# Performance work log

Measured on AMD Instinct MI355X. Metric: run time of the kernel, lower is better.

The kernel has to match this reference:

```python
import jax, jax.numpy as jnp
import numpy as np

BS, SEQ, DIM, HEADS = 2, 2048, 1024, 16
HEAD_DIM = DIM // HEADS
NEG = -1e9


def setup_inputs() -> dict:
    key = jax.random.key(0)
    ks = jax.random.split(key, 5)
    s = 1.0 / np.sqrt(DIM)
    return {
        "x": jax.random.normal(ks[0], (BS, SEQ, DIM), jnp.float32),
        "padding_mask": jnp.ones((BS, SEQ), jnp.int32),
        "causal_mask": jnp.tril(jnp.ones((SEQ, SEQ), jnp.int32)),
        "Wq": jax.random.normal(ks[1], (DIM, DIM), jnp.float32) * s,
        "bq": jnp.zeros((DIM,), jnp.float32),
        "Wk": jax.random.normal(ks[2], (DIM, DIM), jnp.float32) * s,
        "bk": jnp.zeros((DIM,), jnp.float32),
        "Wv": jax.random.normal(ks[3], (DIM, DIM), jnp.float32) * s,
        "bv": jnp.zeros((DIM,), jnp.float32),
        "Wo": jax.random.normal(ks[4], (DIM, DIM), jnp.float32) * s,
        "bo": jnp.zeros((DIM,), jnp.float32),
    }


def reference(x, padding_mask, causal_mask, Wq, bq, Wk, bk, Wv, bv, Wo, bo):
    bs, seq, dim = x.shape
    # QKV projections -> [b, h, s, d]
    def proj(W, b):
        return (x @ W.T + b).reshape(bs, seq, HEADS, HEAD_DIM).transpose(0, 2, 1, 3)
    q, k, v = proj(Wq, bq), proj(Wk, bk), proj(Wv, bv)
    scores = jnp.einsum("bhqd,bhkd->bhqk", q, k) / np.sqrt(HEAD_DIM).astype(np.float32)
    scores = jnp.where(padding_mask[:, None, None, :] == 0, NEG, scores)
    scores = jnp.where(causal_mask[None, None, :, :] == 0, NEG, scores)
    attn = jax.nn.softmax(scores, axis=-1)
    out = jnp.einsum("bhqk,bhkd->bhqd", attn, v)
    out = out.transpose(0, 2, 1, 3).reshape(bs, seq, dim)
    return out @ Wo.T + bo
```

## Files before the change

### kernel.cpp

```cpp
#include <hip/hip_runtime.h>
#include <hip/hip_bf16.h>
#include <stdint.h>

#define SEQ 2048
#define DIM 1024
#define HEADS 16
#define HD 64
#define NEGV (-1e9f)
#define SCALE2 0.18033688011112042f
#define THR2 11.541560327111707f

typedef __attribute__((ext_vector_type(8))) short short8;
typedef __attribute__((ext_vector_type(4))) float f32x4;

__device__ __forceinline__ unsigned short f2bf(float f) {
  __hip_bfloat16 h = __float2bfloat16(f);
  union { __hip_bfloat16 h; unsigned short u; } cv;
  cv.h = h;
  return cv.u;
}

__device__ __forceinline__ void async16(const void* g, void* l) {
  __builtin_amdgcn_global_load_lds(
      (const __attribute__((address_space(1))) unsigned int*)g,
      (__attribute__((address_space(3))) unsigned int*)l, 16, 0, 0);
}

__global__ void cast_bf16_k(const float* __restrict__ in,
                            unsigned short* __restrict__ out, int n4) {
  int stride = gridDim.x * blockDim.x;
  for (int i = blockIdx.x * blockDim.x + threadIdx.x; i < n4; i += stride) {
    float4 v = ((const float4*)in)[i];
    ushort4 o;
    o.x = f2bf(v.x); o.y = f2bf(v.y); o.z = f2bf(v.z); o.w = f2bf(v.w);
    ((ushort4*)out)[i] = o;
  }
}

__global__ void cast_w4_k(const float* __restrict__ w0, const float* __restrict__ w1,
                          const float* __restrict__ w2, const float* __restrict__ w3,
                          unsigned short* __restrict__ o0, unsigned short* __restrict__ o1,
                          unsigned short* __restrict__ o2, unsigned short* __restrict__ o3,
                          int n4) {
  const float* in = (blockIdx.y == 0) ? w0 : (blockIdx.y == 1) ? w1
                   : (blockIdx.y == 2) ? w2 : w3;
  unsigned short* out = (blockIdx.y == 0) ? o0 : (blockIdx.y == 1) ? o1
                       : (blockIdx.y == 2) ? o2 : o3;
  int stride = gridDim.x * blockDim.x;
  for (int i = blockIdx.x * blockDim.x + threadIdx.x; i < n4; i += stride) {
    float4 v = ((const float4*)in)[i];
    ushort4 o;
    o.x = f2bf(v.x); o.y = f2bf(v.y); o.z = f2bf(v.z); o.w = f2bf(v.w);
    ((ushort4*)out)[i] = o;
  }
}

__device__ __forceinline__ void stage_ab(const unsigned short* __restrict__ A,
                                         const unsigned short* __restrict__ B,
                                         int K, int bm0, int bn0, int k0,
                                         unsigned short* As, unsigned short* Bs,
                                         int tid) {
#pragma unroll
  for (int i = 0; i < 2; ++i) {
    int e   = (i * 256 + tid) * 8;
    int row = e >> 5;
    int kk  = e & 31;
    async16(A + (size_t)(bm0 + row) * K + (size_t)(k0 + kk), As + e);
    async16(B + (size_t)(bn0 + row) * K + (size_t)(k0 + kk), Bs + e);
  }
}

__device__ __forceinline__ void gemm_core(const unsigned short* __restrict__ A,
                                          const unsigned short* __restrict__ B,
                                          int K, int bm0, int bn0,
                                          unsigned short (*As)[128 * 32],
                                          unsigned short (*Bs)[128 * 32],
                                          f32x4 acc[4][4]) {
  const int tid  = threadIdx.x;
  const int lane = tid & 63;
  const int w    = tid >> 6;
  const int wr   = w >> 1, wc = w & 1;
  const int lrow = lane & 15, lkg = lane >> 4;

  stage_ab(A, B, K, bm0, bn0, 0, As[0], Bs[0], tid);
  __syncthreads();

  for (int k0 = 0; k0 < K; k0 += 32) {
    const int cur = (k0 >> 5) & 1;
    if (k0 + 32 < K)
      stage_ab(A, B, K, bm0, bn0, k0 + 32, As[cur ^ 1], Bs[cur ^ 1], tid);

    short8 af[4], bf[4];
#pragma unroll
    for (int i = 0; i < 4; ++i) {
      af[i] = *(const short8*)(As[cur] + (wr * 64 + i * 16 + lrow) * 32 + lkg * 8);
      bf[i] = *(const short8*)(Bs[cur] + (wc * 64 + i * 16 + lrow) * 32 + lkg * 8);
    }
#pragma unroll
    for (int i = 0; i < 4; ++i)
#pragma unroll
      for (int j = 0; j < 4; ++j)
        acc[i][j] = __builtin_amdgcn_mfma_f32_16x16x32_bf16(af[i], bf[j], acc[i][j], 0, 0, 0);

    __syncthreads();
  }
}

__global__ __launch_bounds__(256)
void qkv_gemm_k(const unsigned short* __restrict__ xb,
                const unsigned short* __restrict__ wqb,
                const unsigned short* __restrict__ wkb,
                const unsigned short* __restrict__ wvb,
                const float* __restrict__ bq, const float* __restrict__ bk,
                const float* __restrict__ bv,
                unsigned short* __restrict__ Qb, unsigned short* __restrict__ Kb,
                unsigned short* __restrict__ Vtb) {
  __shared__ __align__(16) unsigned short As[2][128 * 32];
  __shared__ __align__(16) unsigned short Bs[2][128 * 32];
  const int z = blockIdx.z;
  const unsigned short* B = (z == 0) ? wqb : (z == 1) ? wkb : wvb;
  const float* bias       = (z == 0) ? bq  : (z == 1) ? bk  : bv;
  const int bm0 = blockIdx.y * 128, bn0 = blockIdx.x * 128;

  f32x4 acc[4][4] = {};
  gemm_core(xb, B, DIM, bm0, bn0, As, Bs, acc);

  const int lane = threadIdx.x & 63;
  const int w = threadIdx.x >> 6, wr = w >> 1, wc = w & 1;
  unsigned short* out01 = (z == 0) ? Qb : Kb;
#pragma unroll
  for (int i = 0; i < 4; ++i)
#pragma unroll
    for (int j = 0; j < 4; ++j)
#pragma unroll
      for (int r = 0; r < 4; ++r) {
        int mg = bm0 + wr * 64 + i * 16 + (lane >> 4) * 4 + r;
        int ng = bn0 + wc * 64 + j * 16 + (lane & 15);
        float v = acc[i][j][r] + bias[ng];
        int bb = mg >> 11, s = mg & 2047, h = ng >> 6, d = ng & 63;
        int bh = bb * HEADS + h;
        if (z < 2)
          out01[((size_t)bh * SEQ + s) * HD + d] = f2bf(v);
        else
          Vtb[((size_t)bh * HD + d) * SEQ + s] = f2bf(v);
      }
}

__global__ __launch_bounds__(256)
void out_gemm_k(const unsigned short* __restrict__ Ob,
                const unsigned short* __restrict__ wob,
                const float* __restrict__ bo, float* __restrict__ out) {
  __shared__ __align__(16) unsigned short As[2][128 * 32];
  __shared__ __align__(16) unsigned short Bs[2][128 * 32];
  const int bm0 = blockIdx.y * 128, bn0 = blockIdx.x * 128;

  f32x4 acc[4][4] = {};
  gemm_core(Ob, wob, DIM, bm0, bn0, As, Bs, acc);

  const int lane = threadIdx.x & 63;
  const int w = threadIdx.x >> 6, wr = w >> 1, wc = w & 1;
#pragma unroll
  for (int i = 0; i < 4; ++i)
#pragma unroll
    for (int j = 0; j < 4; ++j)
#pragma unroll
      for (int r = 0; r < 4; ++r) {
        int mg = bm0 + wr * 64 + i * 16 + (lane >> 4) * 4 + r;
        int ng = bn0 + wc * 64 + j * 16 + (lane & 15);
        out[(size_t)mg * DIM + ng] = acc[i][j][r] + bo[ng];
      }
}

__device__ __forceinline__ void stage_kv64(const unsigned short* __restrict__ kbase,
                                           const unsigned short* __restrict__ vbase,
                                           int k0, unsigned short* KsB,
                                           unsigned short* VsB, int tid) {
#pragma unroll
  for (int j = 0; j < 2; ++j) {
    const int c    = j * 256 + tid;
    const int row  = c >> 3;
    const int colb = (c & 7) << 4;
    const int srcb = colb ^ ((row & 7) << 4);
    async16(kbase + (size_t)(k0 + row) * HD + (srcb >> 1), KsB + c * 8);
  }
#pragma unroll
  for (int j = 0; j < 2; ++j) {
    const int c    = j * 256 + tid;
    const int d    = c >> 3;
    const int colb = (c & 7) << 4;
    const int srcb = colb ^ ((d & 7) << 4);
    async16(vbase + (size_t)d * SEQ + k0 + (srcb >> 1), VsB + c * 8);
  }
}

__global__ __launch_bounds__(256)
void attn_k(const unsigned short* __restrict__ Q,
            const unsigned short* __restrict__ Kp,
            const unsigned short* __restrict__ Vt,
            const int* __restrict__ pm,
            unsigned short* __restrict__ O) {
  __shared__ __align__(16) unsigned short Ks[2][64 * 64];
  __shared__ __align__(16) unsigned short Vs[2][64 * 64];
  __shared__ __align__(16) unsigned short plds[4][16 * 64];

  const int tid  = threadIdx.x;
  const int lane = tid & 63;
  const int w    = tid >> 6;
  const int lc = lane & 15, lg = lane >> 4;
  const int y = blockIdx.y;
  const int r_ = y & 7, m_ = y >> 3;
  const int qb = (m_ == 0) ? r_ : (m_ == 1) ? (15 - r_)
               : (m_ == 2) ? (16 + r_) : (31 - r_);
  const int bh = blockIdx.x;
  const int b  = bh >> 4, h = bh & 15;

  const size_t base = (size_t)bh * SEQ * HD;
  const unsigned short* kbase = Kp + base;
  const unsigned short* vbase = Vt + (size_t)bh * HD * SEQ;
  const int* pmb = pm + b * SEQ;
  char* pb = (char*)&plds[w][0];
  const int swp = (lc & 7) << 4;

  const int qrow0 = qb * 64 + w * 16;
  const int qrow  = qrow0 + lc;

  short8 qa[2];
  {
    const unsigned short* qp = Q + base + (size_t)qrow * HD + lg * 8;
    qa[0] = *(const short8*)(qp);
    qa[1] = *(const short8*)(qp + 32);
  }

  f32x4 oacc[4] = {};
  float mrow = -1e30f, lsum = 0.f;

  const int nk = qb + 1;

  stage_kv64(kbase, vbase, 0, Ks[0], Vs[0], tid);

  int ok = 1;
  for (int i = lane; i < SEQ / 4; i += 64) {
    int4 v = ((const int4*)pmb)[i];
    ok &= (v.x != 0) & (v.y != 0) & (v.z != 0) & (v.w != 0);
  }
  const bool allones = __all(ok);
  __syncthreads();

  for (int kt = 0; kt < nk; ++kt) {
    const int cur = kt & 1;
    const int k0 = kt * 64;
    if (kt + 1 < nk)
      stage_kv64(kbase, vbase, k0 + 64, Ks[cur ^ 1], Vs[cur ^ 1], tid);

    f32x4 s[4];
    const char* kbuf = (const char*)Ks[cur];
    __builtin_amdgcn_s_setprio(1);
#pragma unroll
    for (int t = 0; t < 4; ++t) {
      const int row = t * 16 + lc;
      const int swk = (row & 7) << 4;
      const char* kr = kbuf + row * 128;
      short8 kb0 = *(const short8*)(kr + ((lg * 16) ^ swk));
      short8 kb1 = *(const short8*)(kr + ((lg * 16 + 64) ^ swk));
      f32x4 z = {};
      z = __builtin_amdgcn_mfma_f32_16x16x32_bf16(kb0, qa[0], z, 0, 0, 0);
      z = __builtin_amdgcn_mfma_f32_16x16x32_bf16(kb1, qa[1], z, 0, 0, 0);
#pragma unroll
      for (int r = 0; r < 4; ++r) s[t][r] = z[r] * SCALE2;
    }
    __builtin_amdgcn_s_setprio(0);

    if (!allones) {
#pragma unroll
      for (int t = 0; t < 4; ++t) {
        const int kr0 = k0 + t * 16;
        int4 pmv = *(const int4*)(pmb + kr0 + lg * 4);
#pragma unroll
        for (int r = 0; r < 4; ++r) {
          const int kidx = kr0 + lg * 4 + r;
          if (kidx > qrow || (&pmv.x)[r] == 0) s[t][r] = NEGV;
        }
      }
    } else if (kt == qb) {
#pragma unroll
      for (int t = 0; t < 4; ++t)
#pragma unroll
        for (int r = 0; r < 4; ++r) {
          const int kidx = k0 + t * 16 + lg * 4 + r;
          if (kidx > qrow) s[t][r] = NEGV;
        }
    }

    float mx = -1e30f;
#pragma unroll
    for (int t = 0; t < 4; ++t)
      mx = fmaxf(mx, fmaxf(fmaxf(s[t][0], s[t][1]), fmaxf(s[t][2], s[t][3])));
    if (!__all(mx <= mrow + THR2)) {
      mx = fmaxf(mx, __shfl_xor(mx, 16, 64));
      mx = fmaxf(mx, __shfl_xor(mx, 32, 64));
      const float mnew = fmaxf(mrow, mx);
      const float sc = exp2f(mrow - mnew);
      lsum *= sc;
      mrow = mnew;
      const float s0 = __shfl(sc, lg * 4 + 0, 64);
      const float s1 = __shfl(sc, lg * 4 + 1, 64);
      const float s2 = __shfl(sc, lg * 4 + 2, 64);
      const float s3 = __shfl(sc, lg * 4 + 3, 64);
#pragma unroll
      for (int t = 0; t < 4; ++t) {
        oacc[t][0] *= s0; oacc[t][1] *= s1; oacc[t][2] *= s2; oacc[t][3] *= s3;
      }
    }
    float sum = 0.f;
#pragma unroll
    for (int t = 0; t < 4; ++t)
#pragma unroll
      for (int r = 0; r < 4; ++r) {
        const float p = exp2f(s[t][r] - mrow);
        s[t][r] = p;
        sum += p;
      }
    lsum += sum;

#pragma unroll
    for (int t = 0; t < 4; ++t) {
      short4 pk;
      pk.x = (short)f2bf(s[t][0]); pk.y = (short)f2bf(s[t][1]);
      pk.z = (short)f2bf(s[t][2]); pk.w = (short)f2bf(s[t][3]);
      const int colb = (t * 16 + lg * 4) * 2;
      *(short4*)(pb + lc * 128 + (colb ^ swp)) = pk;
    }
    short8 pa[2];
#pragma unroll
    for (int ks = 0; ks < 2; ++ks)
      pa[ks] = *(const short8*)(pb + lc * 128 + (((ks * 32 + lg * 8) * 2) ^ swp));

    const char* vbuf = (const char*)Vs[cur];
    __builtin_amdgcn_s_setprio(1);
#pragma unroll
    for (int t = 0; t < 4; ++t) {
      const int d = t * 16 + lc;
      const int swv = (d & 7) << 4;
      const char* vr = vbuf + d * 128;
#pragma unroll
      for (int ks = 0; ks < 2; ++ks) {
        short8 vv = *(const short8*)(vr + ((ks * 64 + lg * 16) ^ swv));
        oacc[t] = __builtin_amdgcn_mfma_f32_16x16x32_bf16(pa[ks], vv, oacc[t], 0, 0, 0);
      }
    }
    __builtin_amdgcn_s_setprio(0);

    __syncthreads();
  }

  lsum += __shfl_xor(lsum, 16, 64);
  lsum += __shfl_xor(lsum, 32, 64);
  const float l0 = __shfl(lsum, lg * 4 + 0, 64);
  const float l1 = __shfl(lsum, lg * 4 + 1, 64);
  const float l2 = __shfl(lsum, lg * 4 + 2, 64);
  const float l3 = __shfl(lsum, lg * 4 + 3, 64);
  const float i0 = 1.f / l0, i1 = 1.f / l1, i2 = 1.f / l2, i3 = 1.f / l3;
#pragma unroll
  for (int t = 0; t < 4; ++t) {
    const size_t o0 = ((size_t)(b * SEQ + qrow0 + lg * 4)) * DIM + h * HD + t * 16 + lc;
    O[o0]           = f2bf(oacc[t][0] * i0);
    O[o0 + DIM]     = f2bf(oacc[t][1] * i1);
    O[o0 + 2 * DIM] = f2bf(oacc[t][2] * i2);
    O[o0 + 3 * DIM] = f2bf(oacc[t][3] * i3);
  }
}

extern "C" void kernel_launch(void* const* d_in, const int* in_sizes, int n_in,
                              void* d_out, int out_size, void* d_ws, size_t ws_size,
                              hipStream_t stream) {
  const float* x  = (const float*)d_in[0];
  const int*   pm = (const int*)d_in[1];
  const float* Wq = (const float*)d_in[3];
  const float* bq = (const float*)d_in[4];
  const float* Wk = (const float*)d_in[5];
  const float* bk = (const float*)d_in[6];
  const float* Wv = (const float*)d_in[7];
  const float* bv = (const float*)d_in[8];
  const float* Wo = (const float*)d_in[9];
  const float* bo = (const float*)d_in[10];

  const size_t NX = (size_t)4096 * 1024;
  const size_t NW = (size_t)1024 * 1024;

  unsigned short* ws  = (unsigned short*)d_ws;
  unsigned short* xb  = ws;
  unsigned short* wqb = xb + NX;
  unsigned short* wkb = wqb + NW;
  unsigned short* wvb = wkb + NW;
  unsigned short* wob = wvb + NW;
  unsigned short* Qb  = wob + NW;
  unsigned short* Kb  = Qb + NX;
  unsigned short* Vtb = Kb + NX;
  unsigned short* Ob  = xb;

  cast_bf16_k<<<dim3(2048), dim3(256), 0, stream>>>(x, xb, (int)(NX / 4));
  cast_w4_k<<<dim3(512, 4), dim3(256), 0, stream>>>(Wq, Wk, Wv, Wo,
                                                    wqb, wkb, wvb, wob,
                                                    (int)(NW / 4));

  qkv_gemm_k<<<dim3(8, 32, 3), dim3(256), 0, stream>>>(xb, wqb, wkb, wvb,
                                                       bq, bk, bv, Qb, Kb, Vtb);

  attn_k<<<dim3(32, 32), dim3(256), 0, stream>>>(Qb, Kb, Vtb, pm, Ob);

  out_gemm_k<<<dim3(8, 32), dim3(256), 0, stream>>>(Ob, wob, bo, (float*)d_out);
}
```

Baseline: 131.7 us.

## Use 128-key attention tiles, merge cast kernels, and reorder query blocks

Attention now stages and processes 128 keys per iteration instead of 64. This roughly halves the loop trips and barriers and gives each wave more MFMA work between syncs. In exchange it doubles LDS for the K/V/P buffers, which can lower occupancy, and it wastes masked compute on the diagonal tile when the query-block index is even. Query blocks are now scheduled heaviest-first (descending) instead of in the interleaved order. The x and weight fp32-to-bf16 casts are merged into one launch to save launch overhead.

```diff
diff --git a/kernel.cpp b/kernel.cpp
--- a/kernel.cpp
+++ b/kernel.cpp
@@ -26,26 +26,19 @@
       (__attribute__((address_space(3))) unsigned int*)l, 16, 0, 0);
 }
 
-__global__ void cast_bf16_k(const float* __restrict__ in,
-                            unsigned short* __restrict__ out, int n4) {
-  int stride = gridDim.x * blockDim.x;
-  for (int i = blockIdx.x * blockDim.x + threadIdx.x; i < n4; i += stride) {
-    float4 v = ((const float4*)in)[i];
-    ushort4 o;
-    o.x = f2bf(v.x); o.y = f2bf(v.y); o.z = f2bf(v.z); o.w = f2bf(v.w);
-    ((ushort4*)out)[i] = o;
-  }
-}
-
-__global__ void cast_w4_k(const float* __restrict__ w0, const float* __restrict__ w1,
-                          const float* __restrict__ w2, const float* __restrict__ w3,
-                          unsigned short* __restrict__ o0, unsigned short* __restrict__ o1,
-                          unsigned short* __restrict__ o2, unsigned short* __restrict__ o3,
-                          int n4) {
-  const float* in = (blockIdx.y == 0) ? w0 : (blockIdx.y == 1) ? w1
-                   : (blockIdx.y == 2) ? w2 : w3;
-  unsigned short* out = (blockIdx.y == 0) ? o0 : (blockIdx.y == 1) ? o1
-                       : (blockIdx.y == 2) ? o2 : o3;
+__global__ void cast_all_k(const float* __restrict__ x,
+                           const float* __restrict__ w0, const float* __restrict__ w1,
+                           const float* __restrict__ w2, const float* __restrict__ w3,
+                           unsigned short* __restrict__ xo,
+                           unsigned short* __restrict__ o0, unsigned short* __restrict__ o1,
+                           unsigned short* __restrict__ o2, unsigned short* __restrict__ o3,
+                           int nx4, int nw4) {
+  const int seg = blockIdx.y;
+  const float* in = (seg == 0) ? x : (seg == 1) ? w0 : (seg == 2) ? w1
+                   : (seg == 3) ? w2 : w3;
+  unsigned short* out = (seg == 0) ? xo : (seg == 1) ? o0 : (seg == 2) ? o1
+                       : (seg == 3) ? o2 : o3;
+  const int n4 = (seg == 0) ? nx4 : nw4;
   int stride = gridDim.x * blockDim.x;
   for (int i = blockIdx.x * blockDim.x + threadIdx.x; i < n4; i += stride) {
     float4 v = ((const float4*)in)[i];
@@ -171,12 +164,12 @@
       }
 }
 
-__device__ __forceinline__ void stage_kv64(const unsigned short* __restrict__ kbase,
-                                           const unsigned short* __restrict__ vbase,
-                                           int k0, unsigned short* KsB,
-                                           unsigned short* VsB, int tid) {
-#pragma unroll
-  for (int j = 0; j < 2; ++j) {
+__device__ __forceinline__ void stage_kv128(const unsigned short* __restrict__ kbase,
+                                            const unsigned short* __restrict__ vbase,
+                                            int k0, unsigned short* KsB,
+                                            unsigned short* VsB, int tid) {
+#pragma unroll
+  for (int j = 0; j < 4; ++j) {
     const int c    = j * 256 + tid;
     const int row  = c >> 3;
     const int colb = (c & 7) << 4;
@@ -184,10 +177,10 @@
     async16(kbase + (size_t)(k0 + row) * HD + (srcb >> 1), KsB + c * 8);
   }
 #pragma unroll
-  for (int j = 0; j < 2; ++j) {
+  for (int j = 0; j < 4; ++j) {
     const int c    = j * 256 + tid;
-    const int d    = c >> 3;
-    const int colb = (c & 7) << 4;
+    const int d    = c >> 4;
+    const int colb = (c & 15) << 4;
     const int srcb = colb ^ ((d & 7) << 4);
     async16(vbase + (size_t)d * SEQ + k0 + (srcb >> 1), VsB + c * 8);
   }
@@ -199,18 +192,15 @@
             const unsigned short* __restrict__ Vt,
             const int* __restrict__ pm,
             unsigned short* __restrict__ O) {
-  __shared__ __align__(16) unsigned short Ks[2][64 * 64];
-  __shared__ __align__(16) unsigned short Vs[2][64 * 64];
-  __shared__ __align__(16) unsigned short plds[4][16 * 64];
+  __shared__ __align__(16) unsigned short Ks[2][128 * 64];
+  __shared__ __align__(16) unsigned short Vs[2][64 * 128];
+  __shared__ __align__(16) unsigned short plds[4][16 * 128];
 
   const int tid  = threadIdx.x;
   const int lane = tid & 63;
   const int w    = tid >> 6;
   const int lc = lane & 15, lg = lane >> 4;
-  const int y = blockIdx.y;
-  const int r_ = y & 7, m_ = y >> 3;
-  const int qb = (m_ == 0) ? r_ : (m_ == 1) ? (15 - r_)
-               : (m_ == 2) ? (16 + r_) : (31 - r_);
+  const int qb = 31 - blockIdx.y;
   const int bh = blockIdx.x;
   const int b  = bh >> 4, h = bh & 15;
 
@@ -234,9 +224,9 @@
   f32x4 oacc[4] = {};
   float mrow = -1e30f, lsum = 0.f;
 
-  const int nk = qb + 1;
-
-  stage_kv64(kbase, vbase, 0, Ks[0], Vs[0], tid);
+  const int nk = (qb + 2) >> 1;
+
+  stage_kv128(kbase, vbase, 0, Ks[0], Vs[0], tid);
 
   int ok = 1;
   for (int i = lane; i < SEQ / 4; i += 64) {
@@ -248,15 +238,15 @@
 
   for (int kt = 0; kt < nk; ++kt) {
     const int cur = kt & 1;
-    const int k0 = kt * 64;
+    const int k0 = kt * 128;
     if (kt + 1 < nk)
-      stage_kv64(kbase, vbase, k0 + 64, Ks[cur ^ 1], Vs[cur ^ 1], tid);
-
-    f32x4 s[4];
+      stage_kv128(kbase, vbase, k0 + 128, Ks[cur ^ 1], Vs[cur ^ 1], tid);
+
+    f32x4 s[8];
     const char* kbuf = (const char*)Ks[cur];
     __builtin_amdgcn_s_setprio(1);
 #pragma unroll
-    for (int t = 0; t < 4; ++t) {
+    for (int t = 0; t < 8; ++t) {
       const int row = t * 16 + lc;
       const int swk = (row & 7) << 4;
       const char* kr = kbuf + row * 128;
@@ -272,7 +262,7 @@
 
     if (!allones) {
 #pragma unroll
-      for (int t = 0; t < 4; ++t) {
+      for (int t = 0; t < 8; ++t) {
         const int kr0 = k0 + t * 16;
         int4 pmv = *(const int4*)(pmb + kr0 + lg * 4);
 #pragma unroll
@@ -281,9 +271,9 @@
           if (kidx > qrow || (&pmv.x)[r] == 0) s[t][r] = NEGV;
         }
       }
-    } else if (kt == qb) {
-#pragma unroll
-      for (int t = 0; t < 4; ++t)
+    } else if (kt == nk - 1) {
+#pragma unroll
+      for (int t = 0; t < 8; ++t)
 #pragma unroll
         for (int r = 0; r < 4; ++r) {
           const int kidx = k0 + t * 16 + lg * 4 + r;
@@ -293,7 +283,7 @@
 
     float mx = -1e30f;
 #pragma unroll
-    for (int t = 0; t < 4; ++t)
+    for (int t = 0; t < 8; ++t)
       mx = fmaxf(mx, fmaxf(fmaxf(s[t][0], s[t][1]), fmaxf(s[t][2], s[t][3])));
     if (!__all(mx <= mrow + THR2)) {
       mx = fmaxf(mx, __shfl_xor(mx, 16, 64));
@@ -313,7 +303,7 @@
     }
     float sum = 0.f;
 #pragma unroll
-    for (int t = 0; t < 4; ++t)
+    for (int t = 0; t < 8; ++t)
 #pragma unroll
       for (int r = 0; r < 4; ++r) {
         const float p = exp2f(s[t][r] - mrow);
@@ -323,17 +313,17 @@
     lsum += sum;
 
 #pragma unroll
-    for (int t = 0; t < 4; ++t) {
+    for (int t = 0; t < 8; ++t) {
       short4 pk;
       pk.x = (short)f2bf(s[t][0]); pk.y = (short)f2bf(s[t][1]);
       pk.z = (short)f2bf(s[t][2]); pk.w = (short)f2bf(s[t][3]);
       const int colb = (t * 16 + lg * 4) * 2;
-      *(short4*)(pb + lc * 128 + (colb ^ swp)) = pk;
-    }
-    short8 pa[2];
-#pragma unroll
-    for (int ks = 0; ks < 2; ++ks)
-      pa[ks] = *(const short8*)(pb + lc * 128 + (((ks * 32 + lg * 8) * 2) ^ swp));
+      *(short4*)(pb + lc * 256 + (colb ^ swp)) = pk;
+    }
+    short8 pa[4];
+#pragma unroll
+    for (int ks = 0; ks < 4; ++ks)
+      pa[ks] = *(const short8*)(pb + lc * 256 + (((ks * 32 + lg * 8) * 2) ^ swp));
 
     const char* vbuf = (const char*)Vs[cur];
     __builtin_amdgcn_s_setprio(1);
@@ -341,9 +331,9 @@
     for (int t = 0; t < 4; ++t) {
       const int d = t * 16 + lc;
       const int swv = (d & 7) << 4;
-      const char* vr = vbuf + d * 128;
-#pragma unroll
-      for (int ks = 0; ks < 2; ++ks) {
+      const char* vr = vbuf + d * 256;
+#pragma unroll
+      for (int ks = 0; ks < 4; ++ks) {
         short8 vv = *(const short8*)(vr + ((ks * 64 + lg * 16) ^ swv));
         oacc[t] = __builtin_amdgcn_mfma_f32_16x16x32_bf16(pa[ks], vv, oacc[t], 0, 0, 0);
       }
@@ -398,10 +388,9 @@
   unsigned short* Vtb = Kb + NX;
   unsigned short* Ob  = xb;
 
-  cast_bf16_k<<<dim3(2048), dim3(256), 0, stream>>>(x, xb, (int)(NX / 4));
-  cast_w4_k<<<dim3(512, 4), dim3(256), 0, stream>>>(Wq, Wk, Wv, Wo,
-                                                    wqb, wkb, wvb, wob,
-                                                    (int)(NW / 4));
+  cast_all_k<<<dim3(1024, 5), dim3(256), 0, stream>>>(
+      x, Wq, Wk, Wv, Wo, xb, wqb, wkb, wvb, wob,
+      (int)(NX / 4), (int)(NW / 4));
 
   qkv_gemm_k<<<dim3(8, 32, 3), dim3(256), 0, stream>>>(xb, wqb, wkb, wvb,
                                                        bq, bk, bv, Qb, Kb, Vtb);
```

Measured after the change: 131.4 us. Within noise of the previous version (-0.2%).

## Split long causal query blocks across two KV halves and merge cast kernels

Applied to the files above, without the earlier changes.

The upper 16 query blocks of each head, which have the most causal key tiles, are now split into two work items that each process half the key range. They write unnormalized partial outputs and their max/sum statistics to scratch space in the output buffer. A new combine kernel rescales and merges the two halves. This is meant to balance work across the grid and shorten the critical path of the attention kernel, at the cost of an extra launch, extra traffic and extra rounding of the partials to bf16. The two separate fp32-to-bf16 cast kernels are also fused into one launch.

```diff
diff --git a/kernel.cpp b/kernel.cpp
--- a/kernel.cpp
+++ b/kernel.cpp
@@ -20,32 +20,31 @@
   return cv.u;
 }
 
+__device__ __forceinline__ float bf2f(unsigned short u) {
+  union { unsigned int i; float f; } cv;
+  cv.i = ((unsigned int)u) << 16;
+  return cv.f;
+}
+
 __device__ __forceinline__ void async16(const void* g, void* l) {
   __builtin_amdgcn_global_load_lds(
       (const __attribute__((address_space(1))) unsigned int*)g,
       (__attribute__((address_space(3))) unsigned int*)l, 16, 0, 0);
 }
 
-__global__ void cast_bf16_k(const float* __restrict__ in,
-                            unsigned short* __restrict__ out, int n4) {
-  int stride = gridDim.x * blockDim.x;
-  for (int i = blockIdx.x * blockDim.x + threadIdx.x; i < n4; i += stride) {
-    float4 v = ((const float4*)in)[i];
-    ushort4 o;
-    o.x = f2bf(v.x); o.y = f2bf(v.y); o.z = f2bf(v.z); o.w = f2bf(v.w);
-    ((ushort4*)out)[i] = o;
-  }
-}
-
-__global__ void cast_w4_k(const float* __restrict__ w0, const float* __restrict__ w1,
-                          const float* __restrict__ w2, const float* __restrict__ w3,
-                          unsigned short* __restrict__ o0, unsigned short* __restrict__ o1,
-                          unsigned short* __restrict__ o2, unsigned short* __restrict__ o3,
-                          int n4) {
-  const float* in = (blockIdx.y == 0) ? w0 : (blockIdx.y == 1) ? w1
-                   : (blockIdx.y == 2) ? w2 : w3;
-  unsigned short* out = (blockIdx.y == 0) ? o0 : (blockIdx.y == 1) ? o1
-                       : (blockIdx.y == 2) ? o2 : o3;
+__global__ void cast_all_k(const float* __restrict__ x,
+                           const float* __restrict__ w0, const float* __restrict__ w1,
+                           const float* __restrict__ w2, const float* __restrict__ w3,
+                           unsigned short* __restrict__ xo,
+                           unsigned short* __restrict__ o0, unsigned short* __restrict__ o1,
+                           unsigned short* __restrict__ o2, unsigned short* __restrict__ o3,
+                           int nx4, int nw4) {
+  const int seg = blockIdx.y;
+  const float* in = (seg == 0) ? x : (seg == 1) ? w0 : (seg == 2) ? w1
+                   : (seg == 3) ? w2 : w3;
+  unsigned short* out = (seg == 0) ? xo : (seg == 1) ? o0 : (seg == 2) ? o1
+                       : (seg == 3) ? o2 : o3;
+  const int n4 = (seg == 0) ? nx4 : nw4;
   int stride = gridDim.x * blockDim.x;
   for (int i = blockIdx.x * blockDim.x + threadIdx.x; i < n4; i += stride) {
     float4 v = ((const float4*)in)[i];
@@ -198,7 +197,9 @@
             const unsigned short* __restrict__ Kp,
             const unsigned short* __restrict__ Vt,
             const int* __restrict__ pm,
-            unsigned short* __restrict__ O) {
+            unsigned short* __restrict__ O,
+            unsigned short* __restrict__ pO,
+            float* __restrict__ pml) {
   __shared__ __align__(16) unsigned short Ks[2][64 * 64];
   __shared__ __align__(16) unsigned short Vs[2][64 * 64];
   __shared__ __align__(16) unsigned short plds[4][16 * 64];
@@ -208,11 +209,23 @@
   const int w    = tid >> 6;
   const int lc = lane & 15, lg = lane >> 4;
   const int y = blockIdx.y;
-  const int r_ = y & 7, m_ = y >> 3;
-  const int qb = (m_ == 0) ? r_ : (m_ == 1) ? (15 - r_)
-               : (m_ == 2) ? (16 + r_) : (31 - r_);
   const int bh = blockIdx.x;
   const int b  = bh >> 4, h = bh & 15;
+
+  int qb, ks, ke;
+  bool split;
+  if (y < 32) {
+    split = true;
+    qb = 31 - (y >> 1);
+    const int nk = qb + 1, hk = nk >> 1;
+    ks = (y & 1) ? hk : 0;
+    ke = (y & 1) ? nk : hk;
+  } else {
+    split = false;
+    qb = 47 - y;
+    ks = 0;
+    ke = qb + 1;
+  }
 
   const size_t base = (size_t)bh * SEQ * HD;
   const unsigned short* kbase = Kp + base;
@@ -233,10 +246,9 @@
 
   f32x4 oacc[4] = {};
   float mrow = -1e30f, lsum = 0.f;
-
-  const int nk = qb + 1;
-
-  stage_kv64(kbase, vbase, 0, Ks[0], Vs[0], tid);
+  const int niter = ke - ks;
+
+  stage_kv64(kbase, vbase, ks * 64, Ks[0], Vs[0], tid);
 
   int ok = 1;
   for (int i = lane; i < SEQ / 4; i += 64) {
@@ -246,10 +258,11 @@
   const bool allones = __all(ok);
   __syncthreads();
 
-  for (int kt = 0; kt < nk; ++kt) {
-    const int cur = kt & 1;
+  for (int i = 0; i < niter; ++i) {
+    const int cur = i & 1;
+    const int kt = ks + i;
     const int k0 = kt * 64;
-    if (kt + 1 < nk)
+    if (i + 1 < niter)
       stage_kv64(kbase, vbase, k0 + 64, Ks[cur ^ 1], Vs[cur ^ 1], tid);
 
     f32x4 s[4];
@@ -332,8 +345,8 @@
     }
     short8 pa[2];
 #pragma unroll
-    for (int ks = 0; ks < 2; ++ks)
-      pa[ks] = *(const short8*)(pb + lc * 128 + (((ks * 32 + lg * 8) * 2) ^ swp));
+    for (int ks2 = 0; ks2 < 2; ++ks2)
+      pa[ks2] = *(const short8*)(pb + lc * 128 + (((ks2 * 32 + lg * 8) * 2) ^ swp));
 
     const char* vbuf = (const char*)Vs[cur];
     __builtin_amdgcn_s_setprio(1);
@@ -343,9 +356,9 @@
       const int swv = (d & 7) << 4;
       const char* vr = vbuf + d * 128;
 #pragma unroll
-      for (int ks = 0; ks < 2; ++ks) {
-        short8 vv = *(const short8*)(vr + ((ks * 64 + lg * 16) ^ swv));
-        oacc[t] = __builtin_amdgcn_mfma_f32_16x16x32_bf16(pa[ks], vv, oacc[t], 0, 0, 0);
+      for (int ks2 = 0; ks2 < 2; ++ks2) {
+        short8 vv = *(const short8*)(vr + ((ks2 * 64 + lg * 16) ^ swv));
+        oacc[t] = __builtin_amdgcn_mfma_f32_16x16x32_bf16(pa[ks2], vv, oacc[t], 0, 0, 0);
       }
     }
     __builtin_amdgcn_s_setprio(0);
@@ -355,19 +368,72 @@
 
   lsum += __shfl_xor(lsum, 16, 64);
   lsum += __shfl_xor(lsum, 32, 64);
-  const float l0 = __shfl(lsum, lg * 4 + 0, 64);
-  const float l1 = __shfl(lsum, lg * 4 + 1, 64);
-  const float l2 = __shfl(lsum, lg * 4 + 2, 64);
-  const float l3 = __shfl(lsum, lg * 4 + 3, 64);
-  const float i0 = 1.f / l0, i1 = 1.f / l1, i2 = 1.f / l2, i3 = 1.f / l3;
-#pragma unroll
-  for (int t = 0; t < 4; ++t) {
-    const size_t o0 = ((size_t)(b * SEQ + qrow0 + lg * 4)) * DIM + h * HD + t * 16 + lc;
-    O[o0]           = f2bf(oacc[t][0] * i0);
-    O[o0 + DIM]     = f2bf(oacc[t][1] * i1);
-    O[o0 + 2 * DIM] = f2bf(oacc[t][2] * i2);
-    O[o0 + 3 * DIM] = f2bf(oacc[t][3] * i3);
-  }
+  if (!split) {
+    const float l0 = __shfl(lsum, lg * 4 + 0, 64);
+    const float l1 = __shfl(lsum, lg * 4 + 1, 64);
+    const float l2 = __shfl(lsum, lg * 4 + 2, 64);
+    const float l3 = __shfl(lsum, lg * 4 + 3, 64);
+    const float i0 = 1.f / l0, i1 = 1.f / l1, i2 = 1.f / l2, i3 = 1.f / l3;
+#pragma unroll
+    for (int t = 0; t < 4; ++t) {
+      const size_t o0 = ((size_t)(b * SEQ + qrow0 + lg * 4)) * DIM + h * HD + t * 16 + lc;
+      O[o0]           = f2bf(oacc[t][0] * i0);
+      O[o0 + DIM]     = f2bf(oacc[t][1] * i1);
+      O[o0 + 2 * DIM] = f2bf(oacc[t][2] * i2);
+      O[o0 + 3 * DIM] = f2bf(oacc[t][3] * i3);
+    }
+  } else {
+    const int p = ((qb - 16) * 32 + bh) * 2 + (y & 1);
+    if (lg == 0) {
+      pml[((size_t)p * 64 + w * 16 + lc) * 2 + 0] = mrow;
+      pml[((size_t)p * 64 + w * 16 + lc) * 2 + 1] = lsum;
+    }
+#pragma unroll
+    for (int t = 0; t < 4; ++t)
+#pragma unroll
+      for (int r = 0; r < 4; ++r)
+        pO[((size_t)p * 64 + w * 16 + lg * 4 + r) * 64 + t * 16 + lc] =
+            f2bf(oacc[t][r]);
+  }
+}
+
+__global__ __launch_bounds__(256)
+void attn_combine_k(const unsigned short* __restrict__ pO,
+                    const float* __restrict__ pml,
+                    unsigned short* __restrict__ Ob) {
+  const int bh = blockIdx.x;
+  const int qb = 16 + blockIdx.y;
+  const int b = bh >> 4, h = bh & 15;
+  const int pbase = ((qb - 16) * 32 + bh) * 2;
+  const int r  = threadIdx.x >> 2;
+  const int cb = (threadIdx.x & 3) * 16;
+
+  const float mA = pml[((size_t)(pbase + 0) * 64 + r) * 2 + 0];
+  const float lA = pml[((size_t)(pbase + 0) * 64 + r) * 2 + 1];
+  const float mB = pml[((size_t)(pbase + 1) * 64 + r) * 2 + 0];
+  const float lB = pml[((size_t)(pbase + 1) * 64 + r) * 2 + 1];
+  const float mN = fmaxf(mA, mB);
+  const float aA = exp2f(mA - mN), aB = exp2f(mB - mN);
+  const float il = 1.f / (lA * aA + lB * aB);
+
+  const unsigned short* rowA = pO + ((size_t)(pbase + 0) * 64 + r) * 64 + cb;
+  const unsigned short* rowB = pO + ((size_t)(pbase + 1) * 64 + r) * 64 + cb;
+  unsigned short* orow = Ob + ((size_t)(b * SEQ + qb * 64 + r)) * DIM + h * HD + cb;
+
+  short8 a0 = *(const short8*)(rowA);
+  short8 a1 = *(const short8*)(rowA + 8);
+  short8 b0 = *(const short8*)(rowB);
+  short8 b1 = *(const short8*)(rowB + 8);
+  short8 o0, o1;
+#pragma unroll
+  for (int j = 0; j < 8; ++j) {
+    o0[j] = (short)f2bf((bf2f((unsigned short)a0[j]) * aA +
+                         bf2f((unsigned short)b0[j]) * aB) * il);
+    o1[j] = (short)f2bf((bf2f((unsigned short)a1[j]) * aA +
+                         bf2f((unsigned short)b1[j]) * aB) * il);
+  }
+  *(short8*)(orow)     = o0;
+  *(short8*)(orow + 8) = o1;
 }
 
 extern "C" void kernel_launch(void* const* d_in, const int* in_sizes, int n_in,
@@ -398,15 +464,19 @@
   unsigned short* Vtb = Kb + NX;
   unsigned short* Ob  = xb;
 
-  cast_bf16_k<<<dim3(2048), dim3(256), 0, stream>>>(x, xb, (int)(NX / 4));
-  cast_w4_k<<<dim3(512, 4), dim3(256), 0, stream>>>(Wq, Wk, Wv, Wo,
-                                                    wqb, wkb, wvb, wob,
-                                                    (int)(NW / 4));
+  unsigned short* pO  = (unsigned short*)d_out;
+  float*          pml = (float*)(pO + (size_t)1024 * 64 * 64);
+
+  cast_all_k<<<dim3(1024, 5), dim3(256), 0, stream>>>(
+      x, Wq, Wk, Wv, Wo, xb, wqb, wkb, wvb, wob,
+      (int)(NX / 4), (int)(NW / 4));
 
   qkv_gemm_k<<<dim3(8, 32, 3), dim3(256), 0, stream>>>(xb, wqb, wkb, wvb,
                                                        bq, bk, bv, Qb, Kb, Vtb);
 
-  attn_k<<<dim3(32, 32), dim3(256), 0, stream>>>(Qb, Kb, Vtb, pm, Ob);
+  attn_k<<<dim3(32, 48), dim3(256), 0, stream>>>(Qb, Kb, Vtb, pm, Ob, pO, pml);
+
+  attn_combine_k<<<dim3(32, 16), dim3(256), 0, stream>>>(pO, pml, Ob);
 
   out_gemm_k<<<dim3(8, 32), dim3(256), 0, stream>>>(Ob, wob, bo, (float*)d_out);
 }
```

New measurement: 129.9 us. About the same (-1.4%).
